# Performance work log

Hardware: AMD Instinct MI355X
Metric: run time of the kernel (lower is better)

The kernel has to match this reference:

```python
import jax, jax.numpy as jnp
import numpy as np

P = 5  # patchsize == stride (non-overlapping)


def unfold_patches(x, p):
    # x: [N, C, H, W] -> [N, L, C, p, p], blocks ordered row-major (matches F.unfold)
    N, C, H, W = x.shape
    x = x.reshape(N, C, H // p, p, W // p, p)
    return x.transpose(0, 2, 4, 1, 3, 5).reshape(N, (H // p) * (W // p), C, p, p)


def fold_patches(pat, H, W, p):
    # [N, L, C, p, p] -> [N, C, H, W]; stride==kernel so F.fold is pure placement (no overlap sums)
    N, L, C, _, _ = pat.shape
    x = pat.reshape(N, H // p, W // p, C, p, p)
    return x.transpose(0, 3, 1, 4, 2, 5).reshape(N, C, H, W)


def gather_scale_concat(fold, idx, gamma):
    # fold: [N, L, C, p, p]; idx: [N, L, 4] int; gamma: [4]
    def gath(k):
        return jnp.take_along_axis(fold, idx[:, :, k][:, :, None, None, None], axis=1)
    # first slot uses patch j itself (not idx[...,0]), per the original loop body
    return jnp.concatenate(
        [gamma[0] * fold, gamma[1] * gath(1), gamma[2] * gath(2), gamma[3] * gath(3)], axis=2)


def conv3x3(x, w, b):
    y = jax.lax.conv_general_dilated(x, w, window_strides=(1, 1), padding='SAME',
                                     dimension_numbers=('NCHW', 'OIHW', 'NCHW'))
    return y + b[None, :, None, None]


def setup_inputs() -> dict:
    key = jax.random.key(0)
    ks = jax.random.split(key, 7)
    N, C, H, W = 4, 32, 300, 300
    L = (H // P) * (W // P)
    x_rgb = jax.random.normal(ks[0], (N, C, H, W), dtype=jnp.float32)
    y_hsi = jax.random.normal(ks[1], (N, C, H, W), dtype=jnp.float32)
    corr = jax.random.randint(ks[2], (2, N, L, 4), 0, L)
    rgb_gamma = jnp.ones((4,), jnp.float32)
    hsi_gamma = jnp.ones((4,), jnp.float32)
    rgb_W = jax.random.normal(ks[3], (C, 4 * C, 3, 3), dtype=jnp.float32) * 0.02
    rgb_b = jnp.zeros((C,), jnp.float32)
    hsi_W = jax.random.normal(ks[4], (C, 4 * C, 3, 3), dtype=jnp.float32) * 0.02
    hsi_b = jnp.zeros((C,), jnp.float32)
    return {'x_rgb': x_rgb, 'y_hsi': y_hsi, 'corr': corr,
            'rgb_gamma': rgb_gamma, 'hsi_gamma': hsi_gamma,
            'rgb_W': rgb_W, 'rgb_b': rgb_b, 'hsi_W': hsi_W, 'hsi_b': hsi_b}


def reference(x_rgb, y_hsi, corr, rgb_gamma, hsi_gamma, rgb_W, rgb_b, hsi_W, hsi_b):
    n_feats = x_rgb.shape[1]
    half = n_feats // 2
    H, W = x_rgb.shape[2], x_rgb.shape[3]
    hsi = jnp.concatenate([x_rgb[:, :half], y_hsi[:, :half]], axis=1)      # [N, n_feats, H, W]
    rgb = jnp.concatenate([x_rgb[:, half:n_feats], y_hsi[:, half:n_feats]], axis=1)
    idx = corr[0]  # [N, L, 4]
    # H, W divisible by P -> calc_padding yields zero padding
    fold_rgb = unfold_patches(rgb, P)  # [N, L, C, p, p]
    fold_hsi = unfold_patches(hsi, P)
    patch_rgb = gather_scale_concat(fold_rgb, idx, rgb_gamma)  # [N, L, 4C, p, p]
    patch_hsi = gather_scale_concat(fold_hsi, idx, hsi_gamma)
    img_rgb = fold_patches(patch_rgb, H, W, P)  # [N, 4C, H, W]
    img_hsi = fold_patches(patch_hsi, H, W, P)
    out_rgb = conv3x3(img_rgb, rgb_W, rgb_b) + rgb
    out_hsi = conv3x3(img_hsi, hsi_W, hsi_b) + hsi
    return (out_rgb, out_hsi)
```

## Files before the change

### kernel.cpp

```cpp
#include <hip/hip_runtime.h>

#define HW        90000
#define OUT_HALF  11520000
#define CPLANE    11520000ull
#define WPACK_OFF  46080000ull
#define ZOFF       46227456
#define WS_NEED    (46227456ull + 64ull)

typedef short short4v __attribute__((ext_vector_type(4)));
typedef short short8 __attribute__((ext_vector_type(8)));
typedef float f32x4  __attribute__((ext_vector_type(4)));
typedef unsigned int u32;

__device__ inline short f2bf(float f) {
    unsigned u = __builtin_bit_cast(unsigned, f);
    u += 0x7fff + ((u >> 16) & 1);
    return (short)(u >> 16);
}
__device__ inline float bf2f(short s) {
    unsigned u = ((unsigned)(unsigned short)s) << 16;
    return __builtin_bit_cast(float, u);
}
__device__ inline void gload16(char* ldst, const char* gsrc) {
    __builtin_amdgcn_global_load_lds(
        (const __attribute__((address_space(1))) u32*)gsrc,
        (__attribute__((address_space(3))) u32*)ldst, 16, 0, 0);
}

__global__ __launch_bounds__(256)
void pack_weights(const float* __restrict__ wR, const float* __restrict__ wH,
                  const float* __restrict__ rg, const float* __restrict__ hg,
                  short* __restrict__ wpack) {
    int id = blockIdx.x * 256 + threadIdx.x;
    if (id >= 73728) return;
    int e    = id & 7;
    int lane = (id >> 3) & 63;
    int h    = (id >> 9) & 1;
    int t    = (id >> 10) % 9;
    int kb   = ((id >> 10) / 9) & 3;
    int conv = id / 36864;
    int co   = h * 16 + (lane & 15);
    int cin  = kb * 32 + (lane >> 4) * 8 + e;
    const float* w = conv ? wH : wR;
    const float* g = conv ? hg : rg;
    wpack[id] = f2bf(w[(co * 128 + cin) * 9 + t] * g[cin >> 5]);
}

__global__ __launch_bounds__(256)
void nchw2nhwc(const float* __restrict__ xrgb, const float* __restrict__ yhsi,
               short* __restrict__ cmb) {
    int wave = threadIdx.x >> 6, lane = threadIdx.x & 63;
    if (lane >= 60) return;
    int y = blockIdx.y * 4 + wave;
    int x = blockIdx.x * 60 + lane;
    int n = blockIdx.z;
    const float* xb = xrgb + n * 32 * HW + y * 300 + x;
    const float* yb = yhsi + n * 32 * HW + y * 300 + x;
    size_t pxo = ((size_t)n * HW + y * 300 + x) * 32;
    short* d0 = cmb + pxo;
    short* d1 = cmb + CPLANE + pxo;
    #pragma unroll
    for (int q = 0; q < 4; ++q) {
        short8 v0, v1;
        #pragma unroll
        for (int e = 0; e < 8; ++e) {
            int c = q * 8 + e;
            v0[e] = f2bf((c < 16) ? xb[(16 + c) * HW] : yb[c * HW]);
            v1[e] = f2bf((c < 16) ? xb[c * HW] : yb[(c - 16) * HW]);
        }
        *(short8*)(d0 + q * 8) = v0;
        *(short8*)(d1 + q * 8) = v1;
    }
}

__global__ __launch_bounds__(256, 3)
void conv_mfma(const char* __restrict__ wsbase, const short* __restrict__ wpack,
               const int* __restrict__ corr,
               const float* __restrict__ bR, const float* __restrict__ bH,
               float* __restrict__ out) {
    __shared__ alignas(16) char lds[2][21504];
    int tile = blockIdx.x;
    int n = blockIdx.y;
    int conv = blockIdx.z;
    int ty = tile / 19, tx = tile - ty * 19;
    int y0 = ty * 16, x0 = tx * 16;
    int tid = threadIdx.x;
    int wave = tid >> 6, lane = tid & 63;

    const short* cmb = (const short*)wsbase + conv * CPLANE + (size_t)n * HW * 32;
    const short* wp  = wpack + conv * 36864;
    int cmb_byte = (int)(conv * (CPLANE * 2)) + n * (HW * 64);

    int soffB[6][4];
    #pragma unroll
    for (int ji = 0; ji < 6; ++ji) {
        int j = wave + ji * 4;
        #pragma unroll
        for (int k = 0; k < 4; ++k) soffB[ji][k] = ZOFF;
        if (j < 21) {
            int off = j * 1024 + lane * 16;
            int pxp = off >> 6;
            int pxl = pxp ^ ((pxp >> 2) & 1);
            int cl  = ((off >> 4) & 3) ^ (pxl & 3);
            int cb  = cl * 16;
            #pragma unroll
            for (int k = 0; k < 4; ++k) soffB[ji][k] = ZOFF + cb;
            if (pxl < 324) {
                int hr = pxl / 18, hc = pxl - hr * 18;
                int gy = y0 + hr - 1, gx = x0 + hc - 1;
                if (gy >= 0 && gy < 300 && gx >= 0 && gx < 300) {
                    int pr = gy / 5, pc = gx / 5;
                    int sj = pr * 60 + pc;
                    int sintra = (gy - pr * 5) * 300 + (gx - pc * 5);
                    const int* scr = corr + (n * 3600 + sj) * 4;
                    int j1 = scr[1], j2 = scr[2], j3 = scr[3];
                    soffB[ji][0] = cmb_byte + ((sj / 60) * 1500 + (sj % 60) * 5 + sintra) * 64 + cb;
                    soffB[ji][1] = cmb_byte + ((j1 / 60) * 1500 + (j1 % 60) * 5 + sintra) * 64 + cb;
                    soffB[ji][2] = cmb_byte + ((j2 / 60) * 1500 + (j2 % 60) * 5 + sintra) * 64 + cb;
                    soffB[ji][3] = cmb_byte + ((j3 / 60) * 1500 + (j3 % 60) * 5 + sintra) * 64 + cb;
                }
            }
        }
    }

    #define STAGE(buf, k)                                                        \
        do {                                                                     \
            _Pragma("unroll")                                                    \
            for (int ji = 0; ji < 6; ++ji) {                                     \
                int j = wave + ji * 4;                                           \
                if (j < 21)                                                      \
                    gload16(&lds[buf][j * 1024], wsbase + soffB[ji][(k)]);       \
            }                                                                    \
        } while (0)

    int l15 = lane & 15, lh = lane >> 4;
    int wr = wave * 4;

    int boff[3][6];
    #pragma unroll
    for (int dxi = 0; dxi < 3; ++dxi)
        #pragma unroll
        for (int rr = 0; rr < 6; ++rr) {
            int hp = (wr + rr) * 18 + (l15 + dxi);
            boff[dxi][rr] = (hp * 64 + lh * 16) ^ ((hp & 7) << 4);
        }

    STAGE(0, 0);
    __syncthreads();

    f32x4 acc[4][2];
    #pragma unroll
    for (int g = 0; g < 4; ++g)
        #pragma unroll
        for (int h = 0; h < 2; ++h)
            acc[g][h] = (f32x4){0.f, 0.f, 0.f, 0.f};

    #pragma unroll
    for (int kb = 0; kb < 4; ++kb) {
        short8 a[3][3][2];
        #pragma unroll
        for (int dxi = 0; dxi < 3; ++dxi)
            #pragma unroll
            for (int dyi = 0; dyi < 3; ++dyi) {
                int t = dyi * 3 + dxi;
                a[dxi][dyi][0] = *(const short8*)(wp + (((kb * 9 + t) * 2 + 0) * 64 + lane) * 8);
                a[dxi][dyi][1] = *(const short8*)(wp + (((kb * 9 + t) * 2 + 1) * 64 + lane) * 8);
            }
        __builtin_amdgcn_sched_barrier(0);
        if (kb == 0) STAGE(1, 1);
        if (kb == 1) STAGE(0, 2);
        if (kb == 2) STAGE(1, 3);
        __builtin_amdgcn_sched_barrier(0);
        const char* base = lds[kb & 1];
        #pragma unroll
        for (int dxi = 0; dxi < 3; ++dxi) {
            short8 b[6];
            #pragma unroll
            for (int rr = 0; rr < 6; ++rr)
                b[rr] = *(const short8*)(base + boff[dxi][rr]);
            #pragma unroll
            for (int g = 0; g < 4; ++g) {
                #pragma unroll
                for (int dyi = 0; dyi < 3; ++dyi) {
                    acc[g][0] = __builtin_amdgcn_mfma_f32_16x16x32_bf16(a[dxi][dyi][0], b[g + dyi], acc[g][0], 0, 0, 0);
                    acc[g][1] = __builtin_amdgcn_mfma_f32_16x16x32_bf16(a[dxi][dyi][1], b[g + dyi], acc[g][1], 0, 0, 0);
                }
            }
        }
        if (kb < 3) __syncthreads();
    }

    const float* bias = conv ? bH : bR;
    float bia[2][4];
    #pragma unroll
    for (int h = 0; h < 2; ++h)
        #pragma unroll
        for (int reg = 0; reg < 4; ++reg)
            bia[h][reg] = bias[h * 16 + lh * 4 + reg];
    #pragma unroll
    for (int g = 0; g < 4; ++g) {
        int gy = y0 + wr + g;
        int gx = x0 + l15;
        if (gy < 300 && gx < 300) {
            int pixo = gy * 300 + gx;
            const short* resp = cmb + (size_t)pixo * 32 + lh * 4;
            #pragma unroll
            for (int h = 0; h < 2; ++h) {
                short4v r = *(const short4v*)(resp + h * 16);
                #pragma unroll
                for (int reg = 0; reg < 4; ++reg) {
                    int co = h * 16 + lh * 4 + reg;
                    out[conv * OUT_HALF + (n * 32 + co) * HW + pixo]
                        = acc[g][h][reg] + bia[h][reg] + bf2f(r[reg]);
                }
            }
        }
    }
    #undef STAGE
}

__global__ __launch_bounds__(256)
void fused_gather_conv(const float* __restrict__ xrgb, const float* __restrict__ yhsi,
                       const int* __restrict__ corr, const float* __restrict__ rgb_gamma,
                       const float* __restrict__ hsi_gamma, const float* __restrict__ wR,
                       const float* __restrict__ bR, const float* __restrict__ wH,
                       const float* __restrict__ bH, float* __restrict__ out) {
    int tid = blockIdx.x * blockDim.x + threadIdx.x;
    if (tid >= 4 * HW) return;
    int n = tid / HW, pix = tid - n * HW;
    int y = pix / 300, x = pix - y * 300;
    const int* idx = corr + n * (3600 * 4);
    const float* xb = xrgb + n * (32 * HW);
    const float* yb = yhsi + n * (32 * HW);
    float accR[32], accH[32];
    #pragma unroll
    for (int i = 0; i < 32; ++i) { accR[i] = 0.f; accH[i] = 0.f; }
    for (int k = 0; k < 4; ++k) {
        float gr = rgb_gamma[k], gh = hsi_gamma[k];
        int off[9];
        #pragma unroll
        for (int t = 0; t < 9; ++t) {
            int dy = t / 3 - 1, dx = t % 3 - 1;
            int yy = y + dy, xx = x + dx;
            int o = -1;
            if (yy >= 0 && yy < 300 && xx >= 0 && xx < 300) {
                int pr = yy / 5, pc = xx / 5;
                int j = pr * 60 + pc;
                int jp = (k == 0) ? j : idx[j * 4 + k];
                o = ((jp / 60) * 5 + (yy - pr * 5)) * 300 + (jp % 60) * 5 + (xx - pc * 5);
            }
            off[t] = o;
        }
        for (int c = 0; c < 32; ++c) {
            const float* srcR = (c < 16) ? (xb + (16 + c) * HW) : (yb + c * HW);
            const float* srcH = (c < 16) ? (xb + c * HW) : (yb + (c - 16) * HW);
            float vr[9], vh[9];
            #pragma unroll
            for (int t = 0; t < 9; ++t) {
                bool vld = off[t] >= 0;
                vr[t] = vld ? gr * srcR[off[t]] : 0.f;
                vh[t] = vld ? gh * srcH[off[t]] : 0.f;
            }
            const float* wRp = wR + (k * 32 + c) * 9;
            const float* wHp = wH + (k * 32 + c) * 9;
            #pragma unroll
            for (int t = 0; t < 9; ++t)
                #pragma unroll
                for (int co = 0; co < 32; ++co) {
                    accR[co] = fmaf(vr[t], wRp[co * 1152 + t], accR[co]);
                    accH[co] = fmaf(vh[t], wHp[co * 1152 + t], accH[co]);
                }
        }
    }
    #pragma unroll
    for (int co = 0; co < 32; ++co) {
        float resR = (co < 16) ? xb[(16 + co) * HW + pix] : yb[co * HW + pix];
        float resH = (co < 16) ? xb[co * HW + pix] : yb[(co - 16) * HW + pix];
        out[(n * 32 + co) * HW + pix]            = accR[co] + bR[co] + resR;
        out[OUT_HALF + (n * 32 + co) * HW + pix] = accH[co] + bH[co] + resH;
    }
}

extern "C" void kernel_launch(void* const* d_in, const int* in_sizes, int n_in,
                              void* d_out, int out_size, void* d_ws, size_t ws_size,
                              hipStream_t stream) {
    const float* xrgb = (const float*)d_in[0];
    const float* yhsi = (const float*)d_in[1];
    const int*   corr = (const int*)d_in[2];
    const float* rg   = (const float*)d_in[3];
    const float* hg   = (const float*)d_in[4];
    const float* wR   = (const float*)d_in[5];
    const float* bR   = (const float*)d_in[6];
    const float* wH   = (const float*)d_in[7];
    const float* bH   = (const float*)d_in[8];
    float* out = (float*)d_out;

    if (ws_size >= WS_NEED) {
        short* cmb   = (short*)d_ws;
        short* wpack = (short*)((char*)d_ws + WPACK_OFF);
        hipMemsetAsync((char*)d_ws + ZOFF, 0, 64, stream);
        hipLaunchKernelGGL(pack_weights, dim3(288), dim3(256), 0, stream, wR, wH, rg, hg, wpack);
        hipLaunchKernelGGL(nchw2nhwc, dim3(5, 75, 4), dim3(256), 0, stream, xrgb, yhsi, cmb);
        hipLaunchKernelGGL(conv_mfma, dim3(361, 4, 2), dim3(256), 0, stream,
                           (const char*)d_ws, wpack, corr, bR, bH, out);
    } else {
        int total = 4 * HW;
        hipLaunchKernelGGL(fused_gather_conv, dim3((total + 255) / 256), dim3(256), 0, stream,
                           xrgb, yhsi, corr, rg, hg, wR, bR, wH, bH, out);
    }
}
```

Measured before the change: 126.0 us.

## Process both convs per block and precompute patch base offsets table

Each conv block now handles both the rgb and hsi convolutions in an 8-phase pipelined loop. It reuses the gather offsets computed once per block, because the second workspace plane sits at a fixed delta. A new pack_jb kernel precomputes per-patch base byte offsets from corr, replacing three scalar corr loads and the div/mod work in the conv prologue with one int4 load. The grid is halved to 361x4 blocks, each doing twice the work, which lowers parallelism and adds an extra epilogue in the middle of the loop.

```diff
diff --git a/kernel.cpp b/kernel.cpp
--- a/kernel.cpp
+++ b/kernel.cpp
@@ -2,13 +2,15 @@
 
 #define HW        90000
 #define OUT_HALF  11520000
-#define CPLANE    11520000ull
-#define WPACK_OFF  46080000ull
-#define ZOFF       46227456
-#define WS_NEED    (46227456ull + 64ull)
+#define ZOFF0      23040000
+#define DELTA      23040064
+#define WPACK_OFF  46080128
+#define JB_OFF     46227584
+#define WS_NEED    46457984ull
 
 typedef short short4v __attribute__((ext_vector_type(4)));
 typedef short short8 __attribute__((ext_vector_type(8)));
+typedef int   int4v  __attribute__((ext_vector_type(4)));
 typedef float f32x4  __attribute__((ext_vector_type(4)));
 typedef unsigned int u32;
 
@@ -47,8 +49,17 @@
 }
 
 __global__ __launch_bounds__(256)
+void pack_jb(const int* __restrict__ corr, int* __restrict__ jb) {
+    int id = blockIdx.x * 256 + threadIdx.x;
+    if (id >= 57600) return;
+    int k = id & 3, j = (id >> 2) % 3600, n = id / 14400;
+    int jp = (k == 0) ? j : corr[(n * 3600 + j) * 4 + k];
+    jb[id] = ((jp / 60) * 1500 + (jp % 60) * 5) * 64;
+}
+
+__global__ __launch_bounds__(256)
 void nchw2nhwc(const float* __restrict__ xrgb, const float* __restrict__ yhsi,
-               short* __restrict__ cmb) {
+               char* __restrict__ ws) {
     int wave = threadIdx.x >> 6, lane = threadIdx.x & 63;
     if (lane >= 60) return;
     int y = blockIdx.y * 4 + wave;
@@ -56,9 +67,9 @@
     int n = blockIdx.z;
     const float* xb = xrgb + n * 32 * HW + y * 300 + x;
     const float* yb = yhsi + n * 32 * HW + y * 300 + x;
-    size_t pxo = ((size_t)n * HW + y * 300 + x) * 32;
-    short* d0 = cmb + pxo;
-    short* d1 = cmb + CPLANE + pxo;
+    size_t pxb = ((size_t)n * HW + y * 300 + x) * 64;
+    short* d0 = (short*)(ws + pxb);
+    short* d1 = (short*)(ws + DELTA + pxb);
     #pragma unroll
     for (int q = 0; q < 4; ++q) {
         short8 v0, v1;
@@ -75,61 +86,58 @@
 
 __global__ __launch_bounds__(256, 3)
 void conv_mfma(const char* __restrict__ wsbase, const short* __restrict__ wpack,
-               const int* __restrict__ corr,
                const float* __restrict__ bR, const float* __restrict__ bH,
                float* __restrict__ out) {
     __shared__ alignas(16) char lds[2][21504];
     int tile = blockIdx.x;
     int n = blockIdx.y;
-    int conv = blockIdx.z;
     int ty = tile / 19, tx = tile - ty * 19;
     int y0 = ty * 16, x0 = tx * 16;
     int tid = threadIdx.x;
     int wave = tid >> 6, lane = tid & 63;
 
-    const short* cmb = (const short*)wsbase + conv * CPLANE + (size_t)n * HW * 32;
-    const short* wp  = wpack + conv * 36864;
-    int cmb_byte = (int)(conv * (CPLANE * 2)) + n * (HW * 64);
+    const int* jbtab = (const int*)(wsbase + JB_OFF);
 
     int soffB[6][4];
     #pragma unroll
     for (int ji = 0; ji < 6; ++ji) {
-        int j = wave + ji * 4;
-        #pragma unroll
-        for (int k = 0; k < 4; ++k) soffB[ji][k] = ZOFF;
-        if (j < 21) {
-            int off = j * 1024 + lane * 16;
+        int j4 = wave + ji * 4;
+        #pragma unroll
+        for (int k = 0; k < 4; ++k) soffB[ji][k] = ZOFF0;
+        if (j4 < 21) {
+            int off = j4 * 1024 + lane * 16;
             int pxp = off >> 6;
             int pxl = pxp ^ ((pxp >> 2) & 1);
             int cl  = ((off >> 4) & 3) ^ (pxl & 3);
             int cb  = cl * 16;
             #pragma unroll
-            for (int k = 0; k < 4; ++k) soffB[ji][k] = ZOFF + cb;
+            for (int k = 0; k < 4; ++k) soffB[ji][k] = ZOFF0 + cb;
             if (pxl < 324) {
                 int hr = pxl / 18, hc = pxl - hr * 18;
                 int gy = y0 + hr - 1, gx = x0 + hc - 1;
                 if (gy >= 0 && gy < 300 && gx >= 0 && gx < 300) {
                     int pr = gy / 5, pc = gx / 5;
-                    int sj = pr * 60 + pc;
-                    int sintra = (gy - pr * 5) * 300 + (gx - pc * 5);
-                    const int* scr = corr + (n * 3600 + sj) * 4;
-                    int j1 = scr[1], j2 = scr[2], j3 = scr[3];
-                    soffB[ji][0] = cmb_byte + ((sj / 60) * 1500 + (sj % 60) * 5 + sintra) * 64 + cb;
-                    soffB[ji][1] = cmb_byte + ((j1 / 60) * 1500 + (j1 % 60) * 5 + sintra) * 64 + cb;
-                    soffB[ji][2] = cmb_byte + ((j2 / 60) * 1500 + (j2 % 60) * 5 + sintra) * 64 + cb;
-                    soffB[ji][3] = cmb_byte + ((j3 / 60) * 1500 + (j3 % 60) * 5 + sintra) * 64 + cb;
+                    int j  = pr * 60 + pc;
+                    int intra = (gy - pr * 5) * 300 + (gx - pc * 5);
+                    int4v jbv = *(const int4v*)(jbtab + (n * 3600 + j) * 4);
+                    int base = n * (HW * 64) + intra * 64 + cb;
+                    soffB[ji][0] = base + jbv[0];
+                    soffB[ji][1] = base + jbv[1];
+                    soffB[ji][2] = base + jbv[2];
+                    soffB[ji][3] = base + jbv[3];
                 }
             }
         }
     }
 
-    #define STAGE(buf, k)                                                        \
+    #define STAGE(buf, k, c)                                                     \
         do {                                                                     \
             _Pragma("unroll")                                                    \
             for (int ji = 0; ji < 6; ++ji) {                                     \
-                int j = wave + ji * 4;                                           \
-                if (j < 21)                                                      \
-                    gload16(&lds[buf][j * 1024], wsbase + soffB[ji][(k)]);       \
+                int j4 = wave + ji * 4;                                          \
+                if (j4 < 21)                                                     \
+                    gload16(&lds[buf][j4 * 1024],                                \
+                            wsbase + (c) * DELTA + soffB[ji][(k)]);              \
             }                                                                    \
         } while (0)
 
@@ -145,7 +153,7 @@
             boff[dxi][rr] = (hp * 64 + lh * 16) ^ ((hp & 7) << 4);
         }
 
-    STAGE(0, 0);
+    STAGE(0, 0, 0);
     __syncthreads();
 
     f32x4 acc[4][2];
@@ -155,8 +163,43 @@
         for (int h = 0; h < 2; ++h)
             acc[g][h] = (f32x4){0.f, 0.f, 0.f, 0.f};
 
-    #pragma unroll
-    for (int kb = 0; kb < 4; ++kb) {
+    #define EPI(c)                                                               \
+        do {                                                                     \
+            const float* bias = (c) ? bH : bR;                                   \
+            float bia[2][4];                                                     \
+            _Pragma("unroll")                                                    \
+            for (int h = 0; h < 2; ++h)                                          \
+                _Pragma("unroll")                                                \
+                for (int reg = 0; reg < 4; ++reg)                                \
+                    bia[h][reg] = bias[h * 16 + lh * 4 + reg];                   \
+            _Pragma("unroll")                                                    \
+            for (int g = 0; g < 4; ++g) {                                        \
+                int gy = y0 + wr + g;                                            \
+                int gx = x0 + l15;                                               \
+                if (gy < 300 && gx < 300) {                                      \
+                    int pixo = gy * 300 + gx;                                    \
+                    const short* resp = (const short*)(wsbase + (c) * DELTA      \
+                        + (size_t)(n * HW + pixo) * 64) + lh * 4;                \
+                    _Pragma("unroll")                                            \
+                    for (int h = 0; h < 2; ++h) {                                \
+                        short4v r = *(const short4v*)(resp + h * 16);            \
+                        _Pragma("unroll")                                        \
+                        for (int reg = 0; reg < 4; ++reg) {                      \
+                            int co = h * 16 + lh * 4 + reg;                      \
+                            out[(c) * OUT_HALF + (n * 32 + co) * HW + pixo]      \
+                                = acc[g][h][reg] + bia[h][reg] + bf2f(r[reg]);   \
+                        }                                                        \
+                    }                                                            \
+                }                                                                \
+            }                                                                    \
+        } while (0)
+
+    #pragma unroll
+    for (int p = 0; p < 8; ++p) {
+        const int c  = p >> 2;
+        const int kb = p & 3;
+        const int buf = p & 1;
+        const short* wp = wpack + c * 36864;
         short8 a[3][3][2];
         #pragma unroll
         for (int dxi = 0; dxi < 3; ++dxi)
@@ -167,11 +210,9 @@
                 a[dxi][dyi][1] = *(const short8*)(wp + (((kb * 9 + t) * 2 + 1) * 64 + lane) * 8);
             }
         __builtin_amdgcn_sched_barrier(0);
-        if (kb == 0) STAGE(1, 1);
-        if (kb == 1) STAGE(0, 2);
-        if (kb == 2) STAGE(1, 3);
+        if (p < 7) STAGE(buf ^ 1, (p + 1) & 3, (p + 1) >> 2);
         __builtin_amdgcn_sched_barrier(0);
-        const char* base = lds[kb & 1];
+        const char* base = lds[buf];
         #pragma unroll
         for (int dxi = 0; dxi < 3; ++dxi) {
             short8 b[6];
@@ -187,35 +228,18 @@
                 }
             }
         }
-        if (kb < 3) __syncthreads();
-    }
-
-    const float* bias = conv ? bH : bR;
-    float bia[2][4];
-    #pragma unroll
-    for (int h = 0; h < 2; ++h)
-        #pragma unroll
-        for (int reg = 0; reg < 4; ++reg)
-            bia[h][reg] = bias[h * 16 + lh * 4 + reg];
-    #pragma unroll
-    for (int g = 0; g < 4; ++g) {
-        int gy = y0 + wr + g;
-        int gx = x0 + l15;
-        if (gy < 300 && gx < 300) {
-            int pixo = gy * 300 + gx;
-            const short* resp = cmb + (size_t)pixo * 32 + lh * 4;
-            #pragma unroll
-            for (int h = 0; h < 2; ++h) {
-                short4v r = *(const short4v*)(resp + h * 16);
+        if (p == 3) {
+            EPI(0);
+            #pragma unroll
+            for (int g = 0; g < 4; ++g)
                 #pragma unroll
-                for (int reg = 0; reg < 4; ++reg) {
-                    int co = h * 16 + lh * 4 + reg;
-                    out[conv * OUT_HALF + (n * 32 + co) * HW + pixo]
-                        = acc[g][h][reg] + bia[h][reg] + bf2f(r[reg]);
-                }
-            }
-        }
-    }
+                for (int h = 0; h < 2; ++h)
+                    acc[g][h] = (f32x4){0.f, 0.f, 0.f, 0.f};
+        }
+        if (p < 7) __syncthreads();
+    }
+    EPI(1);
+    #undef EPI
     #undef STAGE
 }
 
@@ -296,13 +320,17 @@
     float* out = (float*)d_out;
 
     if (ws_size >= WS_NEED) {
-        short* cmb   = (short*)d_ws;
-        short* wpack = (short*)((char*)d_ws + WPACK_OFF);
-        hipMemsetAsync((char*)d_ws + ZOFF, 0, 64, stream);
-        hipLaunchKernelGGL(pack_weights, dim3(288), dim3(256), 0, stream, wR, wH, rg, hg, wpack);
-        hipLaunchKernelGGL(nchw2nhwc, dim3(5, 75, 4), dim3(256), 0, stream, xrgb, yhsi, cmb);
-        hipLaunchKernelGGL(conv_mfma, dim3(361, 4, 2), dim3(256), 0, stream,
-                           (const char*)d_ws, wpack, corr, bR, bH, out);
+        char* ws = (char*)d_ws;
+        hipMemsetAsync(ws + ZOFF0, 0, 64, stream);
+        hipMemsetAsync(ws + ZOFF0 + DELTA, 0, 64, stream);
+        hipLaunchKernelGGL(pack_weights, dim3(288), dim3(256), 0, stream,
+                           wR, wH, rg, hg, (short*)(ws + WPACK_OFF));
+        hipLaunchKernelGGL(pack_jb, dim3(225), dim3(256), 0, stream,
+                           corr, (int*)(ws + JB_OFF));
+        hipLaunchKernelGGL(nchw2nhwc, dim3(5, 75, 4), dim3(256), 0, stream,
+                           xrgb, yhsi, ws);
+        hipLaunchKernelGGL(conv_mfma, dim3(361, 4), dim3(256), 0, stream,
+                           (const char*)ws, (const short*)(ws + WPACK_OFF), bR, bH, out);
     } else {
         int total = 4 * HW;
         hipLaunchKernelGGL(fused_gather_conv, dim3((total + 255) / 256), dim3(256), 0, stream,
```

New measurement: 187.0 us. 1.48x slower.
